# Kernel optimization log

Hardware: AMD Instinct MI355X
Metric: run time of the kernel (lower is better)

## Reference

```python
import jax, jax.numpy as jnp
import numpy as np


def setup_inputs() -> dict:
    key = jax.random.key(0)
    ks = jax.random.split(key, 5)
    b, f, h, w, c = 2, 16, 64, 64, 256
    heads, D = 8, 32
    hD = heads * D
    x = jax.random.normal(ks[0], (b, f, h, w, c), dtype=jnp.float32)
    s = 1.0 / np.sqrt(c)
    Wq = jax.random.normal(ks[1], (c, hD), dtype=jnp.float32) * s
    Wk = jax.random.normal(ks[2], (c, hD), dtype=jnp.float32) * s
    Wv = jax.random.normal(ks[3], (c, hD), dtype=jnp.float32) * s
    Wo = jax.random.normal(ks[4], (hD, c), dtype=jnp.float32) * s
    return {"x": x, "Wq": Wq, "Wk": Wk, "Wv": Wv, "Wo": Wo, "heads": heads}


def reference(x, Wq, Wk, Wv, Wo, heads):
    b, f, h, w, c = x.shape
    hD = Wq.shape[1]
    D = hD // heads
    n = h * w
    # fuse batch & frames; 1x1 conv == channel matmul
    xf = x.reshape(b * f, n, c)  # [(bf), n, c]

    def proj(W):
        # [(bf), n, hD] -> [(bf), heads, D, n]
        p = jnp.einsum('bnc,cd->bnd', xf, W)
        return p.reshape(b * f, n, heads, D).transpose(0, 2, 3, 1)

    q = jax.nn.softmax(proj(Wq), axis=-2)  # softmax over D (note: scale is dead code in source)
    k = jax.nn.softmax(proj(Wk), axis=-1)  # softmax over spatial n
    v = proj(Wv)
    context = jnp.einsum('bhdn,bhen->bhde', k, v)      # [(bf), heads, D, D]
    out = jnp.einsum('bhde,bhdn->bhen', context, q)    # [(bf), heads, D, n]
    out = out.transpose(0, 3, 1, 2).reshape(b * f, n, hD)
    out = jnp.einsum('bnd,dc->bnc', out, Wo)
    return out.reshape(b, f, h, w, c)
```

## Files before the change

kernel.cpp:

```cpp
#include <hip/hip_runtime.h>
#include <hip/hip_bf16.h>


typedef __attribute__((ext_vector_type(8))) short bf16x8;
typedef __attribute__((ext_vector_type(4))) float f32x4;

__device__ __forceinline__ unsigned short f2bf(float x) {
  __hip_bfloat16 h = __float2bfloat16(x);
  union { __hip_bfloat16 b; unsigned short u; } c; c.b = h; return c.u;
}

__global__ __launch_bounds__(256) void k0_prep(const float* __restrict__ Wq,
                                               const float* __restrict__ Wk,
                                               const float* __restrict__ Wv,
                                               unsigned short* __restrict__ WqT,
                                               unsigned short* __restrict__ WkvT) {
  int r = blockIdx.x, c = threadIdx.x;
  if (r < 256)      WqT [(r      )*256 + c] = f2bf(Wq[c*256 + r]);
  else if (r < 512) WkvT[(r - 256)*256 + c] = f2bf(Wk[c*256 + (r-256)]);
  else              WkvT[(r - 256)*256 + c] = f2bf(Wv[c*256 + (r-512)]);
}

__global__ __launch_bounds__(512, 2) void k1p(const float* __restrict__ x,
                                              const unsigned short* __restrict__ WkvT,
                                              float* __restrict__ ctxp) {
  __shared__ unsigned short As[2][32*256];
  __shared__ unsigned short slab[512*32];
  int bid = blockIdx.x;
  size_t rowbase = (size_t)bid * 256;
  int tid = threadIdx.x;
  int lane = tid & 63, wid = tid >> 6;
  int cl = lane & 15, rq = (lane >> 4) << 2, fs = lane >> 4;

  bf16x8 bfr[4][8];
#pragma unroll
  for (int nf = 0; nf < 4; ++nf)
#pragma unroll
    for (int kk = 0; kk < 8; ++kk)
      bfr[nf][kk] = *(const bf16x8*)(WkvT + (size_t)(wid*64 + nf*16 + cl)*256 + kk*32 + fs*8);

  f32x4 c2a = {}, c2b = {}, c2c = {}, c2d = {};
  f32x4 c3a = {}, c3b = {};
  bf16x8 bone;
#pragma unroll
  for (int j = 0; j < 8; ++j) bone[j] = (short)0x3F80;

  int ar = tid >> 5, as_ = tid & 31;
  int aw0 = ar*256 + ((as_ ^ (ar & 7)) << 3);
  int aw1 = (16 + ar)*256 + ((as_ ^ (ar & 7)) << 3);
  const float* ap = x + (rowbase + ar)*256 + as_*8;

  float4 pa0 = *(const float4*)ap;
  float4 pa1 = *(const float4*)(ap + 4);
  float4 pa2 = *(const float4*)(ap + 16*256);
  float4 pa3 = *(const float4*)(ap + 16*256 + 4);

  for (int t = 0; t < 8; ++t) {
    unsigned short* Ab = &As[t & 1][0];
    {
      union { ushort4 u4[2]; int4 i4; } pk;
      pk.u4[0].x = f2bf(pa0.x); pk.u4[0].y = f2bf(pa0.y); pk.u4[0].z = f2bf(pa0.z); pk.u4[0].w = f2bf(pa0.w);
      pk.u4[1].x = f2bf(pa1.x); pk.u4[1].y = f2bf(pa1.y); pk.u4[1].z = f2bf(pa1.z); pk.u4[1].w = f2bf(pa1.w);
      *(int4*)(&Ab[aw0]) = pk.i4;
      pk.u4[0].x = f2bf(pa2.x); pk.u4[0].y = f2bf(pa2.y); pk.u4[0].z = f2bf(pa2.z); pk.u4[0].w = f2bf(pa2.w);
      pk.u4[1].x = f2bf(pa3.x); pk.u4[1].y = f2bf(pa3.y); pk.u4[1].z = f2bf(pa3.z); pk.u4[1].w = f2bf(pa3.w);
      *(int4*)(&Ab[aw1]) = pk.i4;
    }
    __syncthreads();
    if (t < 7) {
      const float* apn = ap + (size_t)(t + 1)*32*256;
      pa0 = *(const float4*)apn;
      pa1 = *(const float4*)(apn + 4);
      pa2 = *(const float4*)(apn + 16*256);
      pa3 = *(const float4*)(apn + 16*256 + 4);
    }
    f32x4 acc0[4] = {};
    f32x4 acc1[4] = {};
#pragma unroll
    for (int kk = 0; kk < 8; ++kk) {
      int so = (((kk*4 + fs) ^ (cl & 7)) << 3);
      bf16x8 a0 = *(const bf16x8*)(&Ab[cl*256 + so]);
      bf16x8 a1 = *(const bf16x8*)(&Ab[(16 + cl)*256 + so]);
#pragma unroll
      for (int ni = 0; ni < 4; ++ni) {
        acc0[ni] = __builtin_amdgcn_mfma_f32_16x16x32_bf16(a0, bfr[ni][kk], acc0[ni], 0, 0, 0);
        acc1[ni] = __builtin_amdgcn_mfma_f32_16x16x32_bf16(a1, bfr[ni][kk], acc1[ni], 0, 0, 0);
      }
    }
#pragma unroll
    for (int ni = 0; ni < 4; ++ni) {
      int c = wid*64 + ni*16 + cl;
      int sw = (c ^ (c >> 2)) & 3;
      ushort4 w0, w1;
      if (wid < 4) {
        w0.x = f2bf(__expf(acc0[ni][0])); w0.y = f2bf(__expf(acc0[ni][1]));
        w0.z = f2bf(__expf(acc0[ni][2])); w0.w = f2bf(__expf(acc0[ni][3]));
        w1.x = f2bf(__expf(acc1[ni][0])); w1.y = f2bf(__expf(acc1[ni][1]));
        w1.z = f2bf(__expf(acc1[ni][2])); w1.w = f2bf(__expf(acc1[ni][3]));
      } else {
        w0.x = f2bf(acc0[ni][0]); w0.y = f2bf(acc0[ni][1]);
        w0.z = f2bf(acc0[ni][2]); w0.w = f2bf(acc0[ni][3]);
        w1.x = f2bf(acc1[ni][0]); w1.y = f2bf(acc1[ni][1]);
        w1.z = f2bf(acc1[ni][2]); w1.w = f2bf(acc1[ni][3]);
      }
      *(ushort4*)(&slab[c*32 + (((rq >> 3) ^ sw) << 3) + (rq & 7)]) = w0;
      *(ushort4*)(&slab[c*32 + ((((16 + rq) >> 3) ^ sw) << 3) + (rq & 7)]) = w1;
    }
    __syncthreads();
    {
      int ca0 = wid*32 + cl,        ca1 = wid*32 + 16 + cl;
      int cb0 = 256 + wid*32 + cl,  cb1 = 256 + wid*32 + 16 + cl;
      bf16x8 af0 = *(const bf16x8*)(&slab[ca0*32 + ((fs ^ ((ca0 ^ (ca0 >> 2)) & 3)) << 3)]);
      bf16x8 af1 = *(const bf16x8*)(&slab[ca1*32 + ((fs ^ ((ca1 ^ (ca1 >> 2)) & 3)) << 3)]);
      bf16x8 bv0 = *(const bf16x8*)(&slab[cb0*32 + ((fs ^ ((cb0 ^ (cb0 >> 2)) & 3)) << 3)]);
      bf16x8 bv1 = *(const bf16x8*)(&slab[cb1*32 + ((fs ^ ((cb1 ^ (cb1 >> 2)) & 3)) << 3)]);
      c2a = __builtin_amdgcn_mfma_f32_16x16x32_bf16(af0, bv0, c2a, 0, 0, 0);
      c2b = __builtin_amdgcn_mfma_f32_16x16x32_bf16(af0, bv1, c2b, 0, 0, 0);
      c2c = __builtin_amdgcn_mfma_f32_16x16x32_bf16(af1, bv0, c2c, 0, 0, 0);
      c2d = __builtin_amdgcn_mfma_f32_16x16x32_bf16(af1, bv1, c2d, 0, 0, 0);
      c3a = __builtin_amdgcn_mfma_f32_16x16x32_bf16(af0, bone, c3a, 0, 0, 0);
      c3b = __builtin_amdgcn_mfma_f32_16x16x32_bf16(af1, bone, c3b, 0, 0, 0);
    }
  }
  float* cp = ctxp + ((size_t)bid*8 + wid)*1056;
#pragma unroll
  for (int r = 0; r < 4; ++r) {
    cp[(rq + r)*33 + cl]            = c2a[r];
    cp[(rq + r)*33 + 16 + cl]       = c2b[r];
    cp[(16 + rq + r)*33 + cl]       = c2c[r];
    cp[(16 + rq + r)*33 + 16 + cl]  = c2d[r];
  }
  if (cl == 0) {
#pragma unroll
    for (int r = 0; r < 4; ++r) {
      cp[(rq + r)*33 + 32]      = c3a[r];
      cp[(16 + rq + r)*33 + 32] = c3b[r];
    }
  }
}

__global__ __launch_bounds__(256) void k2b_w2(const float* __restrict__ ctxp,
                                              const float* __restrict__ Wo,
                                              unsigned short* __restrict__ W2t) {
  __shared__ float clds[32*33];
  int bid = blockIdx.x;
  int h = bid & 7, bfi = bid >> 3;
  int tid = threadIdx.x;
  for (int i = tid; i < 1056; i += 256) {
    float s = 0.f;
#pragma unroll
    for (int p = 0; p < 16; ++p)
      s += ctxp[((size_t)(bfi*16 + p)*8 + h)*1056 + i];
    clds[i] = s;
  }
  __syncthreads();
  float acc[32] = {};
#pragma unroll 4
  for (int e = 0; e < 32; ++e) {
    float w = Wo[(size_t)(h*32 + e)*256 + tid];
#pragma unroll
    for (int d = 0; d < 32; ++d) acc[d] += clds[d*33 + e] * w;
  }
  unsigned short* o = W2t + ((size_t)bfi*256 + tid)*256 + h*32;
#pragma unroll
  for (int d = 0; d < 32; ++d) o[d] = f2bf(acc[d] / clds[d*33 + 32]);
}

__global__ __launch_bounds__(512, 2) void k3s(const float* __restrict__ x,
                                              const unsigned short* __restrict__ WqT,
                                              const unsigned short* __restrict__ W2t,
                                              float* __restrict__ out) {
  __shared__ unsigned short As[2][32*256];
  __shared__ unsigned short Qs[2][32*256];
  int bid = blockIdx.x;
  size_t rowbase = (size_t)bid * 256;
  int bfi = bid >> 4;
  int tid = threadIdx.x;
  int lane = tid & 63, wid = tid >> 6;
  int cl = lane & 15, rq = (lane >> 4) << 2, fs = lane >> 4;

  bf16x8 bq[2][8], bw[2][8];
#pragma unroll
  for (int nf = 0; nf < 2; ++nf)
#pragma unroll
    for (int kk = 0; kk < 8; ++kk) {
      bq[nf][kk] = *(const bf16x8*)(WqT + (size_t)(wid*32 + nf*16 + cl)*256 + kk*32 + fs*8);
      bw[nf][kk] = *(const bf16x8*)(W2t + ((size_t)bfi*256 + wid*32 + nf*16 + cl)*256 + kk*32 + fs*8);
    }

  int ar = tid >> 5, as_ = tid & 31;
  int aw0 = ar*256 + ((as_ ^ (ar & 7)) << 3);
  int aw1 = (16 + ar)*256 + ((as_ ^ (ar & 7)) << 3);
  const float* ap = x + (rowbase + ar)*256 + as_*8;

  int qslotbase = wid*4 + (rq >> 3);
  ushort4 qpk[2][2];

  float4 pa0 = *(const float4*)ap;
  float4 pa1 = *(const float4*)(ap + 4);
  float4 pa2 = *(const float4*)(ap + 16*256);
  float4 pa3 = *(const float4*)(ap + 16*256 + 4);
  {
    unsigned short* Ab = &As[0][0];
    union { ushort4 u4[2]; int4 i4; } pk;
    pk.u4[0].x = f2bf(pa0.x); pk.u4[0].y = f2bf(pa0.y); pk.u4[0].z = f2bf(pa0.z); pk.u4[0].w = f2bf(pa0.w);
    pk.u4[1].x = f2bf(pa1.x); pk.u4[1].y = f2bf(pa1.y); pk.u4[1].z = f2bf(pa1.z); pk.u4[1].w = f2bf(pa1.w);
    *(int4*)(&Ab[aw0]) = pk.i4;
    pk.u4[0].x = f2bf(pa2.x); pk.u4[0].y = f2bf(pa2.y); pk.u4[0].z = f2bf(pa2.z); pk.u4[0].w = f2bf(pa2.w);
    pk.u4[1].x = f2bf(pa3.x); pk.u4[1].y = f2bf(pa3.y); pk.u4[1].z = f2bf(pa3.z); pk.u4[1].w = f2bf(pa3.w);
    *(int4*)(&Ab[aw1]) = pk.i4;
  }
  {
    const float* apn = ap + 32*256;
    pa0 = *(const float4*)apn;
    pa1 = *(const float4*)(apn + 4);
    pa2 = *(const float4*)(apn + 16*256);
    pa3 = *(const float4*)(apn + 16*256 + 4);
  }
  __syncthreads();
  {
    unsigned short* Ab = &As[0][0];
    f32x4 ql[2][2] = {};
#pragma unroll
    for (int kk = 0; kk < 8; ++kk) {
      int so = (((kk*4 + fs) ^ (cl & 7)) << 3);
      bf16x8 a0 = *(const bf16x8*)(&Ab[cl*256 + so]);
      bf16x8 a1 = *(const bf16x8*)(&Ab[(16 + cl)*256 + so]);
#pragma unroll
      for (int nf = 0; nf < 2; ++nf) {
        ql[0][nf] = __builtin_amdgcn_mfma_f32_16x16x32_bf16(bq[nf][kk], a0, ql[0][nf], 0, 0, 0);
        ql[1][nf] = __builtin_amdgcn_mfma_f32_16x16x32_bf16(bq[nf][kk], a1, ql[1][nf], 0, 0, 0);
      }
    }
#pragma unroll
    for (int m = 0; m < 2; ++m) {
      float e0[4], e1[4]; float s8 = 0.f;
#pragma unroll
      for (int r = 0; r < 4; ++r) { e0[r] = __expf(ql[m][0][r]); e1[r] = __expf(ql[m][1][r]); s8 += e0[r] + e1[r]; }
      float s = s8; s += __shfl_xor(s, 16); s += __shfl_xor(s, 32);
      float inv = 1.0f / s;
      qpk[m][0].x = f2bf(e0[0]*inv); qpk[m][0].y = f2bf(e0[1]*inv); qpk[m][0].z = f2bf(e0[2]*inv); qpk[m][0].w = f2bf(e0[3]*inv);
      qpk[m][1].x = f2bf(e1[0]*inv); qpk[m][1].y = f2bf(e1[1]*inv); qpk[m][1].z = f2bf(e1[2]*inv); qpk[m][1].w = f2bf(e1[3]*inv);
    }
  }
  for (int t = 0; t < 7; ++t) {
    {
      unsigned short* Ab = &As[(t + 1) & 1][0];
      union { ushort4 u4[2]; int4 i4; } pk;
      pk.u4[0].x = f2bf(pa0.x); pk.u4[0].y = f2bf(pa0.y); pk.u4[0].z = f2bf(pa0.z); pk.u4[0].w = f2bf(pa0.w);
      pk.u4[1].x = f2bf(pa1.x); pk.u4[1].y = f2bf(pa1.y); pk.u4[1].z = f2bf(pa1.z); pk.u4[1].w = f2bf(pa1.w);
      *(int4*)(&Ab[aw0]) = pk.i4;
      pk.u4[0].x = f2bf(pa2.x); pk.u4[0].y = f2bf(pa2.y); pk.u4[0].z = f2bf(pa2.z); pk.u4[0].w = f2bf(pa2.w);
      pk.u4[1].x = f2bf(pa3.x); pk.u4[1].y = f2bf(pa3.y); pk.u4[1].z = f2bf(pa3.z); pk.u4[1].w = f2bf(pa3.w);
      *(int4*)(&Ab[aw1]) = pk.i4;
    }
    {
      unsigned short* Qb = &Qs[t & 1][0];
#pragma unroll
      for (int m = 0; m < 2; ++m) {
        int row = m*16 + cl;
#pragma unroll
        for (int nf = 0; nf < 2; ++nf) {
          int slot = qslotbase + nf*2;
          *(ushort4*)(&Qb[row*256 + ((slot ^ (row & 7)) << 3) + (rq & 4)]) = qpk[m][nf];
        }
      }
    }
    if (t < 6) {
      const float* apn = ap + (size_t)(t + 2)*32*256;
      pa0 = *(const float4*)apn;
      pa1 = *(const float4*)(apn + 4);
      pa2 = *(const float4*)(apn + 16*256);
      pa3 = *(const float4*)(apn + 16*256 + 4);
    }
    __syncthreads();
    f32x4 oa[2][2] = {};
    {
      unsigned short* Qb = &Qs[t & 1][0];
#pragma unroll
      for (int kk = 0; kk < 8; ++kk) {
        int so = (((kk*4 + fs) ^ (cl & 7)) << 3);
        bf16x8 q0 = *(const bf16x8*)(&Qb[cl*256 + so]);
        bf16x8 q1 = *(const bf16x8*)(&Qb[(16 + cl)*256 + so]);
#pragma unroll
        for (int nf = 0; nf < 2; ++nf) {
          oa[0][nf] = __builtin_amdgcn_mfma_f32_16x16x32_bf16(bw[nf][kk], q0, oa[0][nf], 0, 0, 0);
          oa[1][nf] = __builtin_amdgcn_mfma_f32_16x16x32_bf16(bw[nf][kk], q1, oa[1][nf], 0, 0, 0);
        }
      }
    }
    {
      unsigned short* Ab = &As[(t + 1) & 1][0];
      f32x4 ql[2][2] = {};
#pragma unroll
      for (int kk = 0; kk < 8; ++kk) {
        int so = (((kk*4 + fs) ^ (cl & 7)) << 3);
        bf16x8 a0 = *(const bf16x8*)(&Ab[cl*256 + so]);
        bf16x8 a1 = *(const bf16x8*)(&Ab[(16 + cl)*256 + so]);
#pragma unroll
        for (int nf = 0; nf < 2; ++nf) {
          ql[0][nf] = __builtin_amdgcn_mfma_f32_16x16x32_bf16(bq[nf][kk], a0, ql[0][nf], 0, 0, 0);
          ql[1][nf] = __builtin_amdgcn_mfma_f32_16x16x32_bf16(bq[nf][kk], a1, ql[1][nf], 0, 0, 0);
        }
      }
#pragma unroll
      for (int m = 0; m < 2; ++m) {
        float e0[4], e1[4]; float s8 = 0.f;
#pragma unroll
        for (int r = 0; r < 4; ++r) { e0[r] = __expf(ql[m][0][r]); e1[r] = __expf(ql[m][1][r]); s8 += e0[r] + e1[r]; }
        float s = s8; s += __shfl_xor(s, 16); s += __shfl_xor(s, 32);
        float inv = 1.0f / s;
        qpk[m][0].x = f2bf(e0[0]*inv); qpk[m][0].y = f2bf(e0[1]*inv); qpk[m][0].z = f2bf(e0[2]*inv); qpk[m][0].w = f2bf(e0[3]*inv);
        qpk[m][1].x = f2bf(e1[0]*inv); qpk[m][1].y = f2bf(e1[1]*inv); qpk[m][1].z = f2bf(e1[2]*inv); qpk[m][1].w = f2bf(e1[3]*inv);
      }
    }
#pragma unroll
    for (int m = 0; m < 2; ++m)
#pragma unroll
      for (int nf = 0; nf < 2; ++nf)
        *(f32x4*)(&out[(rowbase + (size_t)t*32 + m*16 + cl)*256 + wid*32 + nf*16 + rq]) = oa[m][nf];
  }
  {
    unsigned short* Qb = &Qs[1][0];
#pragma unroll
    for (int m = 0; m < 2; ++m) {
      int row = m*16 + cl;
#pragma unroll
      for (int nf = 0; nf < 2; ++nf) {
        int slot = qslotbase + nf*2;
        *(ushort4*)(&Qb[row*256 + ((slot ^ (row & 7)) << 3) + (rq & 4)]) = qpk[m][nf];
      }
    }
  }
  __syncthreads();
  {
    unsigned short* Qb = &Qs[1][0];
    f32x4 oa[2][2] = {};
#pragma unroll
    for (int kk = 0; kk < 8; ++kk) {
      int so = (((kk*4 + fs) ^ (cl & 7)) << 3);
      bf16x8 q0 = *(const bf16x8*)(&Qb[cl*256 + so]);
      bf16x8 q1 = *(const bf16x8*)(&Qb[(16 + cl)*256 + so]);
#pragma unroll
      for (int nf = 0; nf < 2; ++nf) {
        oa[0][nf] = __builtin_amdgcn_mfma_f32_16x16x32_bf16(bw[nf][kk], q0, oa[0][nf], 0, 0, 0);
        oa[1][nf] = __builtin_amdgcn_mfma_f32_16x16x32_bf16(bw[nf][kk], q1, oa[1][nf], 0, 0, 0);
      }
    }
#pragma unroll
    for (int m = 0; m < 2; ++m)
#pragma unroll
      for (int nf = 0; nf < 2; ++nf)
        *(f32x4*)(&out[(rowbase + (size_t)7*32 + m*16 + cl)*256 + wid*32 + nf*16 + rq]) = oa[m][nf];
  }
}

extern "C" void kernel_launch(void* const* d_in, const int* in_sizes, int n_in,
                              void* d_out, int out_size, void* d_ws, size_t ws_size,
                              hipStream_t stream) {
  const float* x  = (const float*)d_in[0];
  const float* Wq = (const float*)d_in[1];
  const float* Wk = (const float*)d_in[2];
  const float* Wv = (const float*)d_in[3];
  const float* Wo = (const float*)d_in[4];
  float* out = (float*)d_out;

  unsigned short* WkvT = (unsigned short*)d_ws;
  unsigned short* WqT  = WkvT + 131072;
  unsigned short* W2t  = WqT  + 65536;
  float*          ctxp = (float*)(W2t + 2097152);

  k0_prep <<<768,  256, 0, stream>>>(Wq, Wk, Wv, WqT, WkvT);
  k1p     <<<512,  512, 0, stream>>>(x, WkvT, ctxp);
  k2b_w2  <<<256,  256, 0, stream>>>(ctxp, Wo, W2t);
  k3s     <<<512,  512, 0, stream>>>(x, WqT, W2t, out);
}
```

Measured before the change: 141.9 us.

## Software-pipeline k1p with double-buffered slab and one barrier per step

Measured after the change: 142.8 us. Within noise of the previous version (+0.6%).

```diff
diff --git a/kernel.cpp b/kernel.cpp
--- a/kernel.cpp
+++ b/kernel.cpp
@@ -25,7 +25,7 @@
                                               const unsigned short* __restrict__ WkvT,
                                               float* __restrict__ ctxp) {
   __shared__ unsigned short As[2][32*256];
-  __shared__ unsigned short slab[512*32];
+  __shared__ unsigned short slab[2][512*32];
   int bid = blockIdx.x;
   size_t rowbase = (size_t)bid * 256;
   int tid = threadIdx.x;
@@ -50,14 +50,79 @@
   int aw1 = (16 + ar)*256 + ((as_ ^ (ar & 7)) << 3);
   const float* ap = x + (rowbase + ar)*256 + as_*8;
 
+  int ca0 = wid*32 + cl,        ca1 = wid*32 + 16 + cl;
+  int cb0 = 256 + wid*32 + cl,  cb1 = 256 + wid*32 + 16 + cl;
+  int ra0 = ca0*32 + ((fs ^ ((ca0 ^ (ca0 >> 2)) & 3)) << 3);
+  int ra1 = ca1*32 + ((fs ^ ((ca1 ^ (ca1 >> 2)) & 3)) << 3);
+  int rb0 = cb0*32 + ((fs ^ ((cb0 ^ (cb0 >> 2)) & 3)) << 3);
+  int rb1 = cb1*32 + ((fs ^ ((cb1 ^ (cb1 >> 2)) & 3)) << 3);
+
+  f32x4 acc0[4], acc1[4];
+
   float4 pa0 = *(const float4*)ap;
   float4 pa1 = *(const float4*)(ap + 4);
   float4 pa2 = *(const float4*)(ap + 16*256);
   float4 pa3 = *(const float4*)(ap + 16*256 + 4);
-
-  for (int t = 0; t < 8; ++t) {
-    unsigned short* Ab = &As[t & 1][0];
-    {
+  {
+    unsigned short* Ab = &As[0][0];
+    union { ushort4 u4[2]; int4 i4; } pk;
+    pk.u4[0].x = f2bf(pa0.x); pk.u4[0].y = f2bf(pa0.y); pk.u4[0].z = f2bf(pa0.z); pk.u4[0].w = f2bf(pa0.w);
+    pk.u4[1].x = f2bf(pa1.x); pk.u4[1].y = f2bf(pa1.y); pk.u4[1].z = f2bf(pa1.z); pk.u4[1].w = f2bf(pa1.w);
+    *(int4*)(&Ab[aw0]) = pk.i4;
+    pk.u4[0].x = f2bf(pa2.x); pk.u4[0].y = f2bf(pa2.y); pk.u4[0].z = f2bf(pa2.z); pk.u4[0].w = f2bf(pa2.w);
+    pk.u4[1].x = f2bf(pa3.x); pk.u4[1].y = f2bf(pa3.y); pk.u4[1].z = f2bf(pa3.z); pk.u4[1].w = f2bf(pa3.w);
+    *(int4*)(&Ab[aw1]) = pk.i4;
+  }
+  {
+    const float* apn = ap + 32*256;
+    pa0 = *(const float4*)apn;
+    pa1 = *(const float4*)(apn + 4);
+    pa2 = *(const float4*)(apn + 16*256);
+    pa3 = *(const float4*)(apn + 16*256 + 4);
+  }
+  __syncthreads();
+  {
+    unsigned short* Ab = &As[0][0];
+#pragma unroll
+    for (int ni = 0; ni < 4; ++ni) { acc0[ni] = (f32x4){}; acc1[ni] = (f32x4){}; }
+#pragma unroll
+    for (int kk = 0; kk < 8; ++kk) {
+      int so = (((kk*4 + fs) ^ (cl & 7)) << 3);
+      bf16x8 a0 = *(const bf16x8*)(&Ab[cl*256 + so]);
+      bf16x8 a1 = *(const bf16x8*)(&Ab[(16 + cl)*256 + so]);
+#pragma unroll
+      for (int ni = 0; ni < 4; ++ni) {
+        acc0[ni] = __builtin_amdgcn_mfma_f32_16x16x32_bf16(a0, bfr[ni][kk], acc0[ni], 0, 0, 0);
+        acc1[ni] = __builtin_amdgcn_mfma_f32_16x16x32_bf16(a1, bfr[ni][kk], acc1[ni], 0, 0, 0);
+      }
+    }
+  }
+
+  for (int t = 0; t < 7; ++t) {
+    {
+      unsigned short* sb = &slab[t & 1][0];
+#pragma unroll
+      for (int ni = 0; ni < 4; ++ni) {
+        int c = wid*64 + ni*16 + cl;
+        int sw = (c ^ (c >> 2)) & 3;
+        ushort4 w0, w1;
+        if (wid < 4) {
+          w0.x = f2bf(__expf(acc0[ni][0])); w0.y = f2bf(__expf(acc0[ni][1]));
+          w0.z = f2bf(__expf(acc0[ni][2])); w0.w = f2bf(__expf(acc0[ni][3]));
+          w1.x = f2bf(__expf(acc1[ni][0])); w1.y = f2bf(__expf(acc1[ni][1]));
+          w1.z = f2bf(__expf(acc1[ni][2])); w1.w = f2bf(__expf(acc1[ni][3]));
+        } else {
+          w0.x = f2bf(acc0[ni][0]); w0.y = f2bf(acc0[ni][1]);
+          w0.z = f2bf(acc0[ni][2]); w0.w = f2bf(acc0[ni][3]);
+          w1.x = f2bf(acc1[ni][0]); w1.y = f2bf(acc1[ni][1]);
+          w1.z = f2bf(acc1[ni][2]); w1.w = f2bf(acc1[ni][3]);
+        }
+        *(ushort4*)(&sb[c*32 + (((rq >> 3) ^ sw) << 3) + (rq & 7)]) = w0;
+        *(ushort4*)(&sb[c*32 + ((((16 + rq) >> 3) ^ sw) << 3) + (rq & 7)]) = w1;
+      }
+    }
+    {
+      unsigned short* Ab = &As[(t + 1) & 1][0];
       union { ushort4 u4[2]; int4 i4; } pk;
       pk.u4[0].x = f2bf(pa0.x); pk.u4[0].y = f2bf(pa0.y); pk.u4[0].z = f2bf(pa0.z); pk.u4[0].w = f2bf(pa0.w);
       pk.u4[1].x = f2bf(pa1.x); pk.u4[1].y = f2bf(pa1.y); pk.u4[1].z = f2bf(pa1.z); pk.u4[1].w = f2bf(pa1.w);
@@ -66,27 +131,46 @@
       pk.u4[1].x = f2bf(pa3.x); pk.u4[1].y = f2bf(pa3.y); pk.u4[1].z = f2bf(pa3.z); pk.u4[1].w = f2bf(pa3.w);
       *(int4*)(&Ab[aw1]) = pk.i4;
     }
-    __syncthreads();
-    if (t < 7) {
-      const float* apn = ap + (size_t)(t + 1)*32*256;
+    if (t < 6) {
+      const float* apn = ap + (size_t)(t + 2)*32*256;
       pa0 = *(const float4*)apn;
       pa1 = *(const float4*)(apn + 4);
       pa2 = *(const float4*)(apn + 16*256);
       pa3 = *(const float4*)(apn + 16*256 + 4);
     }
-    f32x4 acc0[4] = {};
-    f32x4 acc1[4] = {};
-#pragma unroll
-    for (int kk = 0; kk < 8; ++kk) {
-      int so = (((kk*4 + fs) ^ (cl & 7)) << 3);
-      bf16x8 a0 = *(const bf16x8*)(&Ab[cl*256 + so]);
-      bf16x8 a1 = *(const bf16x8*)(&Ab[(16 + cl)*256 + so]);
-#pragma unroll
-      for (int ni = 0; ni < 4; ++ni) {
-        acc0[ni] = __builtin_amdgcn_mfma_f32_16x16x32_bf16(a0, bfr[ni][kk], acc0[ni], 0, 0, 0);
-        acc1[ni] = __builtin_amdgcn_mfma_f32_16x16x32_bf16(a1, bfr[ni][kk], acc1[ni], 0, 0, 0);
-      }
-    }
+    __syncthreads();
+    {
+      unsigned short* sb = &slab[t & 1][0];
+      bf16x8 af0 = *(const bf16x8*)(&sb[ra0]);
+      bf16x8 af1 = *(const bf16x8*)(&sb[ra1]);
+      bf16x8 bv0 = *(const bf16x8*)(&sb[rb0]);
+      bf16x8 bv1 = *(const bf16x8*)(&sb[rb1]);
+      c2a = __builtin_amdgcn_mfma_f32_16x16x32_bf16(af0, bv0, c2a, 0, 0, 0);
+      c2b = __builtin_amdgcn_mfma_f32_16x16x32_bf16(af0, bv1, c2b, 0, 0, 0);
+      c2c = __builtin_amdgcn_mfma_f32_16x16x32_bf16(af1, bv0, c2c, 0, 0, 0);
+      c2d = __builtin_amdgcn_mfma_f32_16x16x32_bf16(af1, bv1, c2d, 0, 0, 0);
+      c3a = __builtin_amdgcn_mfma_f32_16x16x32_bf16(af0, bone, c3a, 0, 0, 0);
+      c3b = __builtin_amdgcn_mfma_f32_16x16x32_bf16(af1, bone, c3b, 0, 0, 0);
+    }
+    {
+      unsigned short* Ab = &As[(t + 1) & 1][0];
+#pragma unroll
+      for (int ni = 0; ni < 4; ++ni) { acc0[ni] = (f32x4){}; acc1[ni] = (f32x4){}; }
+#pragma unroll
+      for (int kk = 0; kk < 8; ++kk) {
+        int so = (((kk*4 + fs) ^ (cl & 7)) << 3);
+        bf16x8 a0 = *(const bf16x8*)(&Ab[cl*256 + so]);
+        bf16x8 a1 = *(const bf16x8*)(&Ab[(16 + cl)*256 + so]);
+#pragma unroll
+        for (int ni = 0; ni < 4; ++ni) {
+          acc0[ni] = __builtin_amdgcn_mfma_f32_16x16x32_bf16(a0, bfr[ni][kk], acc0[ni], 0, 0, 0);
+          acc1[ni] = __builtin_amdgcn_mfma_f32_16x16x32_bf16(a1, bfr[ni][kk], acc1[ni], 0, 0, 0);
+        }
+      }
+    }
+  }
+  {
+    unsigned short* sb = &slab[1][0];
 #pragma unroll
     for (int ni = 0; ni < 4; ++ni) {
       int c = wid*64 + ni*16 + cl;
@@ -103,24 +187,23 @@
         w1.x = f2bf(acc1[ni][0]); w1.y = f2bf(acc1[ni][1]);
         w1.z = f2bf(acc1[ni][2]); w1.w = f2bf(acc1[ni][3]);
       }
-      *(ushort4*)(&slab[c*32 + (((rq >> 3) ^ sw) << 3) + (rq & 7)]) = w0;
-      *(ushort4*)(&slab[c*32 + ((((16 + rq) >> 3) ^ sw) << 3) + (rq & 7)]) = w1;
-    }
-    __syncthreads();
-    {
-      int ca0 = wid*32 + cl,        ca1 = wid*32 + 16 + cl;
-      int cb0 = 256 + wid*32 + cl,  cb1 = 256 + wid*32 + 16 + cl;
-      bf16x8 af0 = *(const bf16x8*)(&slab[ca0*32 + ((fs ^ ((ca0 ^ (ca0 >> 2)) & 3)) << 3)]);
-      bf16x8 af1 = *(const bf16x8*)(&slab[ca1*32 + ((fs ^ ((ca1 ^ (ca1 >> 2)) & 3)) << 3)]);
-      bf16x8 bv0 = *(const bf16x8*)(&slab[cb0*32 + ((fs ^ ((cb0 ^ (cb0 >> 2)) & 3)) << 3)]);
-      bf16x8 bv1 = *(const bf16x8*)(&slab[cb1*32 + ((fs ^ ((cb1 ^ (cb1 >> 2)) & 3)) << 3)]);
-      c2a = __builtin_amdgcn_mfma_f32_16x16x32_bf16(af0, bv0, c2a, 0, 0, 0);
-      c2b = __builtin_amdgcn_mfma_f32_16x16x32_bf16(af0, bv1, c2b, 0, 0, 0);
-      c2c = __builtin_amdgcn_mfma_f32_16x16x32_bf16(af1, bv0, c2c, 0, 0, 0);
-      c2d = __builtin_amdgcn_mfma_f32_16x16x32_bf16(af1, bv1, c2d, 0, 0, 0);
-      c3a = __builtin_amdgcn_mfma_f32_16x16x32_bf16(af0, bone, c3a, 0, 0, 0);
-      c3b = __builtin_amdgcn_mfma_f32_16x16x32_bf16(af1, bone, c3b, 0, 0, 0);
-    }
+      *(ushort4*)(&sb[c*32 + (((rq >> 3) ^ sw) << 3) + (rq & 7)]) = w0;
+      *(ushort4*)(&sb[c*32 + ((((16 + rq) >> 3) ^ sw) << 3) + (rq & 7)]) = w1;
+    }
+  }
+  __syncthreads();
+  {
+    unsigned short* sb = &slab[1][0];
+    bf16x8 af0 = *(const bf16x8*)(&sb[ra0]);
+    bf16x8 af1 = *(const bf16x8*)(&sb[ra1]);
+    bf16x8 bv0 = *(const bf16x8*)(&sb[rb0]);
+    bf16x8 bv1 = *(const bf16x8*)(&sb[rb1]);
+    c2a = __builtin_amdgcn_mfma_f32_16x16x32_bf16(af0, bv0, c2a, 0, 0, 0);
+    c2b = __builtin_amdgcn_mfma_f32_16x16x32_bf16(af0, bv1, c2b, 0, 0, 0);
+    c2c = __builtin_amdgcn_mfma_f32_16x16x32_bf16(af1, bv0, c2c, 0, 0, 0);
+    c2d = __builtin_amdgcn_mfma_f32_16x16x32_bf16(af1, bv1, c2d, 0, 0, 0);
+    c3a = __builtin_amdgcn_mfma_f32_16x16x32_bf16(af0, bone, c3a, 0, 0, 0);
+    c3b = __builtin_amdgcn_mfma_f32_16x16x32_bf16(af1, bone, c3b, 0, 0, 0);
   }
   float* cp = ctxp + ((size_t)bid*8 + wid)*1056;
 #pragma unroll
```

## Split K/V projection across heads, cache bf16 x for Q pass via LDS DMA

Applied to the files above, without the earlier changes.

Measured after the change: 202.1 us. 1.42x slower.

```diff
diff --git a/kernel.cpp b/kernel.cpp
--- a/kernel.cpp
+++ b/kernel.cpp
@@ -8,6 +8,11 @@
 __device__ __forceinline__ unsigned short f2bf(float x) {
   __hip_bfloat16 h = __float2bfloat16(x);
   union { __hip_bfloat16 b; unsigned short u; } c; c.b = h; return c.u;
+}
+
+__device__ __forceinline__ void gl16(const unsigned short* g, unsigned short* l) {
+  __builtin_amdgcn_global_load_lds((const __attribute__((address_space(1))) void*)g,
+                                   (__attribute__((address_space(3))) void*)l, 16, 0, 0);
 }
 
 __global__ __launch_bounds__(256) void k0_prep(const float* __restrict__ Wq,
@@ -21,120 +26,148 @@
   else              WkvT[(r - 256)*256 + c] = f2bf(Wv[c*256 + (r-512)]);
 }
 
-__global__ __launch_bounds__(512, 2) void k1p(const float* __restrict__ x,
+__global__ __launch_bounds__(512, 4) void k1x(const float* __restrict__ x,
                                               const unsigned short* __restrict__ WkvT,
-                                              float* __restrict__ ctxp) {
+                                              float* __restrict__ ctxp,
+                                              unsigned short* __restrict__ XB) {
   __shared__ unsigned short As[2][32*256];
-  __shared__ unsigned short slab[512*32];
+  __shared__ unsigned short slab[2][256*32];
   int bid = blockIdx.x;
-  size_t rowbase = (size_t)bid * 256;
+  int rc = bid & 511, hb = bid >> 9;
+  size_t rowbase = (size_t)rc * 256;
   int tid = threadIdx.x;
-  int lane = tid & 63, wid = tid >> 6;
+  int lane = tid & 63, w = tid >> 6;
   int cl = lane & 15, rq = (lane >> 4) << 2, fs = lane >> 4;
-
-  bf16x8 bfr[4][8];
-#pragma unroll
-  for (int nf = 0; nf < 4; ++nf)
+  bool isE = w < 4;
+  int wb = isE ? hb*128 + w*32 : 256 + hb*128 + (w - 4)*32;
+
+  bf16x8 bfr[2][8];
+#pragma unroll
+  for (int ni = 0; ni < 2; ++ni)
 #pragma unroll
     for (int kk = 0; kk < 8; ++kk)
-      bfr[nf][kk] = *(const bf16x8*)(WkvT + (size_t)(wid*64 + nf*16 + cl)*256 + kk*32 + fs*8);
-
-  f32x4 c2a = {}, c2b = {}, c2c = {}, c2d = {};
-  f32x4 c3a = {}, c3b = {};
-  bf16x8 bone;
-#pragma unroll
-  for (int j = 0; j < 8; ++j) bone[j] = (short)0x3F80;
+      bfr[ni][kk] = *(const bf16x8*)(WkvT + (size_t)(wb + ni*16 + cl)*256 + kk*32 + fs*8);
+
+  int hl = w >> 1, dh = w & 1;
+  f32x4 c2[2] = {};
+  float dena0 = 0.f, dena1 = 0.f;
 
   int ar = tid >> 5, as_ = tid & 31;
   int aw0 = ar*256 + ((as_ ^ (ar & 7)) << 3);
   int aw1 = (16 + ar)*256 + ((as_ ^ (ar & 7)) << 3);
   const float* ap = x + (rowbase + ar)*256 + as_*8;
-
-  float4 pa0 = *(const float4*)ap;
-  float4 pa1 = *(const float4*)(ap + 4);
-  float4 pa2 = *(const float4*)(ap + 16*256);
-  float4 pa3 = *(const float4*)(ap + 16*256 + 4);
-
-  for (int t = 0; t < 8; ++t) {
-    unsigned short* Ab = &As[t & 1][0];
-    {
-      union { ushort4 u4[2]; int4 i4; } pk;
-      pk.u4[0].x = f2bf(pa0.x); pk.u4[0].y = f2bf(pa0.y); pk.u4[0].z = f2bf(pa0.z); pk.u4[0].w = f2bf(pa0.w);
-      pk.u4[1].x = f2bf(pa1.x); pk.u4[1].y = f2bf(pa1.y); pk.u4[1].z = f2bf(pa1.z); pk.u4[1].w = f2bf(pa1.w);
-      *(int4*)(&Ab[aw0]) = pk.i4;
-      pk.u4[0].x = f2bf(pa2.x); pk.u4[0].y = f2bf(pa2.y); pk.u4[0].z = f2bf(pa2.z); pk.u4[0].w = f2bf(pa2.w);
-      pk.u4[1].x = f2bf(pa3.x); pk.u4[1].y = f2bf(pa3.y); pk.u4[1].z = f2bf(pa3.z); pk.u4[1].w = f2bf(pa3.w);
-      *(int4*)(&Ab[aw1]) = pk.i4;
-    }
-    __syncthreads();
-    if (t < 7) {
-      const float* apn = ap + (size_t)(t + 1)*32*256;
-      pa0 = *(const float4*)apn;
-      pa1 = *(const float4*)(apn + 4);
-      pa2 = *(const float4*)(apn + 16*256);
-      pa3 = *(const float4*)(apn + 16*256 + 4);
-    }
-    f32x4 acc0[4] = {};
-    f32x4 acc1[4] = {};
+  unsigned short* xbp = XB + (rowbase + ar)*256 + as_*8;
+
+  int ca  = hl*32 + dh*16 + cl;
+  int cb0 = 128 + hl*32 + cl, cb1 = cb0 + 16;
+  int ra  = ca*32  + ((fs ^ ((ca ^ (ca >> 2)) & 3)) << 3);
+  int rb0 = cb0*32 + ((fs ^ ((cb0 ^ (cb0 >> 2)) & 3)) << 3);
+  int rb1 = cb1*32 + ((fs ^ ((cb1 ^ (cb1 >> 2)) & 3)) << 3);
+
+  f32x4 acc[2][2];
+  float4 pa0, pa1, pa2, pa3;
+
+  auto loadpa = [&](int ts) {
+    const float* p = ap + (size_t)ts*32*256;
+    pa0 = *(const float4*)p;
+    pa1 = *(const float4*)(p + 4);
+    pa2 = *(const float4*)(p + 16*256);
+    pa3 = *(const float4*)(p + 16*256 + 4);
+  };
+  auto stage = [&](int buf, int ts) {
+    unsigned short* Ab = &As[buf][0];
+    union { ushort4 u4[2]; int4 i4; } pk;
+    pk.u4[0].x = f2bf(pa0.x); pk.u4[0].y = f2bf(pa0.y); pk.u4[0].z = f2bf(pa0.z); pk.u4[0].w = f2bf(pa0.w);
+    pk.u4[1].x = f2bf(pa1.x); pk.u4[1].y = f2bf(pa1.y); pk.u4[1].z = f2bf(pa1.z); pk.u4[1].w = f2bf(pa1.w);
+    *(int4*)(&Ab[aw0]) = pk.i4;
+    if (hb == 0) *(int4*)(xbp + (size_t)ts*8192) = pk.i4;
+    pk.u4[0].x = f2bf(pa2.x); pk.u4[0].y = f2bf(pa2.y); pk.u4[0].z = f2bf(pa2.z); pk.u4[0].w = f2bf(pa2.w);
+    pk.u4[1].x = f2bf(pa3.x); pk.u4[1].y = f2bf(pa3.y); pk.u4[1].z = f2bf(pa3.z); pk.u4[1].w = f2bf(pa3.w);
+    *(int4*)(&Ab[aw1]) = pk.i4;
+    if (hb == 0) *(int4*)(xbp + (size_t)ts*8192 + 4096) = pk.i4;
+  };
+  auto mainmfma = [&](int buf) {
+    unsigned short* Ab = &As[buf][0];
+#pragma unroll
+    for (int m = 0; m < 2; ++m)
+#pragma unroll
+      for (int ni = 0; ni < 2; ++ni) acc[m][ni] = (f32x4){};
 #pragma unroll
     for (int kk = 0; kk < 8; ++kk) {
       int so = (((kk*4 + fs) ^ (cl & 7)) << 3);
       bf16x8 a0 = *(const bf16x8*)(&Ab[cl*256 + so]);
       bf16x8 a1 = *(const bf16x8*)(&Ab[(16 + cl)*256 + so]);
 #pragma unroll
-      for (int ni = 0; ni < 4; ++ni) {
-        acc0[ni] = __builtin_amdgcn_mfma_f32_16x16x32_bf16(a0, bfr[ni][kk], acc0[ni], 0, 0, 0);
-        acc1[ni] = __builtin_amdgcn_mfma_f32_16x16x32_bf16(a1, bfr[ni][kk], acc1[ni], 0, 0, 0);
-      }
-    }
-#pragma unroll
-    for (int ni = 0; ni < 4; ++ni) {
-      int c = wid*64 + ni*16 + cl;
+      for (int ni = 0; ni < 2; ++ni) {
+        acc[0][ni] = __builtin_amdgcn_mfma_f32_16x16x32_bf16(a0, bfr[ni][kk], acc[0][ni], 0, 0, 0);
+        acc[1][ni] = __builtin_amdgcn_mfma_f32_16x16x32_bf16(a1, bfr[ni][kk], acc[1][ni], 0, 0, 0);
+      }
+    }
+  };
+  auto slabwrite = [&](int buf) {
+    unsigned short* sb = &slab[buf][0];
+#pragma unroll
+    for (int ni = 0; ni < 2; ++ni) {
+      int c = w*32 + ni*16 + cl;
       int sw = (c ^ (c >> 2)) & 3;
-      ushort4 w0, w1;
-      if (wid < 4) {
-        w0.x = f2bf(__expf(acc0[ni][0])); w0.y = f2bf(__expf(acc0[ni][1]));
-        w0.z = f2bf(__expf(acc0[ni][2])); w0.w = f2bf(__expf(acc0[ni][3]));
-        w1.x = f2bf(__expf(acc1[ni][0])); w1.y = f2bf(__expf(acc1[ni][1]));
-        w1.z = f2bf(__expf(acc1[ni][2])); w1.w = f2bf(__expf(acc1[ni][3]));
-      } else {
-        w0.x = f2bf(acc0[ni][0]); w0.y = f2bf(acc0[ni][1]);
-        w0.z = f2bf(acc0[ni][2]); w0.w = f2bf(acc0[ni][3]);
-        w1.x = f2bf(acc1[ni][0]); w1.y = f2bf(acc1[ni][1]);
-        w1.z = f2bf(acc1[ni][2]); w1.w = f2bf(acc1[ni][3]);
-      }
-      *(ushort4*)(&slab[c*32 + (((rq >> 3) ^ sw) << 3) + (rq & 7)]) = w0;
-      *(ushort4*)(&slab[c*32 + ((((16 + rq) >> 3) ^ sw) << 3) + (rq & 7)]) = w1;
-    }
+#pragma unroll
+      for (int m = 0; m < 2; ++m) {
+        int n4 = m*16 + rq;
+        ushort4 wv;
+        if (isE) {
+          float e0 = __expf(acc[m][ni][0]), e1 = __expf(acc[m][ni][1]);
+          float e2 = __expf(acc[m][ni][2]), e3 = __expf(acc[m][ni][3]);
+          if (ni == 0) dena0 += (e0 + e1) + (e2 + e3); else dena1 += (e0 + e1) + (e2 + e3);
+          wv.x = f2bf(e0); wv.y = f2bf(e1); wv.z = f2bf(e2); wv.w = f2bf(e3);
+        } else {
+          wv.x = f2bf(acc[m][ni][0]); wv.y = f2bf(acc[m][ni][1]);
+          wv.z = f2bf(acc[m][ni][2]); wv.w = f2bf(acc[m][ni][3]);
+        }
+        *(ushort4*)(&sb[c*32 + (((n4 >> 3) ^ sw) << 3) + (n4 & 7)]) = wv;
+      }
+    }
+  };
+  auto ctxmfma = [&](int buf) {
+    unsigned short* sb = &slab[buf][0];
+    bf16x8 af  = *(const bf16x8*)(&sb[ra]);
+    bf16x8 bv0 = *(const bf16x8*)(&sb[rb0]);
+    bf16x8 bv1 = *(const bf16x8*)(&sb[rb1]);
+    c2[0] = __builtin_amdgcn_mfma_f32_16x16x32_bf16(af, bv0, c2[0], 0, 0, 0);
+    c2[1] = __builtin_amdgcn_mfma_f32_16x16x32_bf16(af, bv1, c2[1], 0, 0, 0);
+  };
+
+  loadpa(0);
+  stage(0, 0);
+  loadpa(1);
+  __syncthreads();
+  mainmfma(0);
+
+  for (int t = 0; t < 7; ++t) {
+    slabwrite(t & 1);
+    stage((t + 1) & 1, t + 1);
+    if (t < 6) loadpa(t + 2);
     __syncthreads();
-    {
-      int ca0 = wid*32 + cl,        ca1 = wid*32 + 16 + cl;
-      int cb0 = 256 + wid*32 + cl,  cb1 = 256 + wid*32 + 16 + cl;
-      bf16x8 af0 = *(const bf16x8*)(&slab[ca0*32 + ((fs ^ ((ca0 ^ (ca0 >> 2)) & 3)) << 3)]);
-      bf16x8 af1 = *(const bf16x8*)(&slab[ca1*32 + ((fs ^ ((ca1 ^ (ca1 >> 2)) & 3)) << 3)]);
-      bf16x8 bv0 = *(const bf16x8*)(&slab[cb0*32 + ((fs ^ ((cb0 ^ (cb0 >> 2)) & 3)) << 3)]);
-      bf16x8 bv1 = *(const bf16x8*)(&slab[cb1*32 + ((fs ^ ((cb1 ^ (cb1 >> 2)) & 3)) << 3)]);
-      c2a = __builtin_amdgcn_mfma_f32_16x16x32_bf16(af0, bv0, c2a, 0, 0, 0);
-      c2b = __builtin_amdgcn_mfma_f32_16x16x32_bf16(af0, bv1, c2b, 0, 0, 0);
-      c2c = __builtin_amdgcn_mfma_f32_16x16x32_bf16(af1, bv0, c2c, 0, 0, 0);
-      c2d = __builtin_amdgcn_mfma_f32_16x16x32_bf16(af1, bv1, c2d, 0, 0, 0);
-      c3a = __builtin_amdgcn_mfma_f32_16x16x32_bf16(af0, bone, c3a, 0, 0, 0);
-      c3b = __builtin_amdgcn_mfma_f32_16x16x32_bf16(af1, bone, c3b, 0, 0, 0);
-    }
-  }
-  float* cp = ctxp + ((size_t)bid*8 + wid)*1056;
-#pragma unroll
-  for (int r = 0; r < 4; ++r) {
-    cp[(rq + r)*33 + cl]            = c2a[r];
-    cp[(rq + r)*33 + 16 + cl]       = c2b[r];
-    cp[(16 + rq + r)*33 + cl]       = c2c[r];
-    cp[(16 + rq + r)*33 + 16 + cl]  = c2d[r];
-  }
-  if (cl == 0) {
-#pragma unroll
-    for (int r = 0; r < 4; ++r) {
-      cp[(rq + r)*33 + 32]      = c3a[r];
-      cp[(16 + rq + r)*33 + 32] = c3b[r];
+    ctxmfma(t & 1);
+    mainmfma((t + 1) & 1);
+  }
+  slabwrite(1);
+  __syncthreads();
+  ctxmfma(1);
+
+  int hgl = hb*4 + hl;
+  float* cp = ctxp + ((size_t)rc*8 + hgl)*1056;
+#pragma unroll
+  for (int eh = 0; eh < 2; ++eh)
+#pragma unroll
+    for (int r = 0; r < 4; ++r)
+      cp[(dh*16 + rq + r)*33 + eh*16 + cl] = c2[eh][r];
+  if (isE) {
+    dena0 += __shfl_xor(dena0, 16); dena0 += __shfl_xor(dena0, 32);
+    dena1 += __shfl_xor(dena1, 16); dena1 += __shfl_xor(dena1, 32);
+    float* cpd = ctxp + ((size_t)rc*8 + hb*4 + w)*1056;
+    if (fs == 0) {
+      cpd[cl*33 + 32]        = dena0;
+      cpd[(16 + cl)*33 + 32] = dena1;
     }
   }
 }
@@ -166,7 +199,7 @@
   for (int d = 0; d < 32; ++d) o[d] = f2bf(acc[d] / clds[d*33 + 32]);
 }
 
-__global__ __launch_bounds__(512, 2) void k3s(const float* __restrict__ x,
+__global__ __launch_bounds__(512, 2) void k3x(const unsigned short* __restrict__ XB,
                                               const unsigned short* __restrict__ WqT,
                                               const unsigned short* __restrict__ W2t,
                                               float* __restrict__ out) {
@@ -188,38 +221,19 @@
       bw[nf][kk] = *(const bf16x8*)(W2t + ((size_t)bfi*256 + wid*32 + nf*16 + cl)*256 + kk*32 + fs*8);
     }
 
-  int ar = tid >> 5, as_ = tid & 31;
-  int aw0 = ar*256 + ((as_ ^ (ar & 7)) << 3);
-  int aw1 = (16 + ar)*256 + ((as_ ^ (ar & 7)) << 3);
-  const float* ap = x + (rowbase + ar)*256 + as_*8;
+  int sr = tid >> 5, ss = tid & 31;
+  const unsigned short* xs0 = XB + (rowbase + sr)*256 + ((ss ^ (sr & 7)) << 3);
+  const unsigned short* xs1 = xs0 + 16*256;
 
   int qslotbase = wid*4 + (rq >> 3);
   ushort4 qpk[2][2];
 
-  float4 pa0 = *(const float4*)ap;
-  float4 pa1 = *(const float4*)(ap + 4);
-  float4 pa2 = *(const float4*)(ap + 16*256);
-  float4 pa3 = *(const float4*)(ap + 16*256 + 4);
-  {
-    unsigned short* Ab = &As[0][0];
-    union { ushort4 u4[2]; int4 i4; } pk;
-    pk.u4[0].x = f2bf(pa0.x); pk.u4[0].y = f2bf(pa0.y); pk.u4[0].z = f2bf(pa0.z); pk.u4[0].w = f2bf(pa0.w);
-    pk.u4[1].x = f2bf(pa1.x); pk.u4[1].y = f2bf(pa1.y); pk.u4[1].z = f2bf(pa1.z); pk.u4[1].w = f2bf(pa1.w);
-    *(int4*)(&Ab[aw0]) = pk.i4;
-    pk.u4[0].x = f2bf(pa2.x); pk.u4[0].y = f2bf(pa2.y); pk.u4[0].z = f2bf(pa2.z); pk.u4[0].w = f2bf(pa2.w);
-    pk.u4[1].x = f2bf(pa3.x); pk.u4[1].y = f2bf(pa3.y); pk.u4[1].z = f2bf(pa3.z); pk.u4[1].w = f2bf(pa3.w);
-    *(int4*)(&Ab[aw1]) = pk.i4;
-  }
-  {
-    const float* apn = ap + 32*256;
-    pa0 = *(const float4*)apn;
-    pa1 = *(const float4*)(apn + 4);
-    pa2 = *(const float4*)(apn + 16*256);
-    pa3 = *(const float4*)(apn + 16*256 + 4);
-  }
-  __syncthreads();
-  {
-    unsigned short* Ab = &As[0][0];
+  auto stageA = [&](int buf, int ts) {
+    gl16(xs0 + (size_t)ts*8192, &As[buf][(wid*64)*8]);
+    gl16(xs1 + (size_t)ts*8192, &As[buf][(512 + wid*64)*8]);
+  };
+  auto p1soft = [&](int buf) {
+    unsigned short* Ab = &As[buf][0];
     f32x4 ql[2][2] = {};
 #pragma unroll
     for (int kk = 0; kk < 8; ++kk) {
@@ -242,37 +256,27 @@
       qpk[m][0].x = f2bf(e0[0]*inv); qpk[m][0].y = f2bf(e0[1]*inv); qpk[m][0].z = f2bf(e0[2]*inv); qpk[m][0].w = f2bf(e0[3]*inv);
       qpk[m][1].x = f2bf(e1[0]*inv); qpk[m][1].y = f2bf(e1[1]*inv); qpk[m][1].z = f2bf(e1[2]*inv); qpk[m][1].w = f2bf(e1[3]*inv);
     }
-  }
+  };
+  auto qwrite = [&](int buf) {
+    unsigned short* Qb = &Qs[buf][0];
+#pragma unroll
+    for (int m = 0; m < 2; ++m) {
+      int row = m*16 + cl;
+#pragma unroll
+      for (int nf = 0; nf < 2; ++nf) {
+        int slot = qslotbase + nf*2;
+        *(ushort4*)(&Qb[row*256 + ((slot ^ (row & 7)) << 3) + (rq & 4)]) = qpk[m][nf];
+      }
+    }
+  };
+
+  stageA(0, 0);
+  __syncthreads();
+  p1soft(0);
+
   for (int t = 0; t < 7; ++t) {
-    {
-      unsigned short* Ab = &As[(t + 1) & 1][0];
-      union { ushort4 u4[2]; int4 i4; } pk;
-      pk.u4[0].x = f2bf(pa0.x); pk.u4[0].y = f2bf(pa0.y); pk.u4[0].z = f2bf(pa0.z); pk.u4[0].w = f2bf(pa0.w);
-      pk.u4[1].x = f2bf(pa1.x); pk.u4[1].y = f2bf(pa1.y); pk.u4[1].z = f2bf(pa1.z); pk.u4[1].w = f2bf(pa1.w);
-      *(int4*)(&Ab[aw0]) = pk.i4;
-      pk.u4[0].x = f2bf(pa2.x); pk.u4[0].y = f2bf(pa2.y); pk.u4[0].z = f2bf(pa2.z); pk.u4[0].w = f2bf(pa2.w);
-      pk.u4[1].x = f2bf(pa3.x); pk.u4[1].y = f2bf(pa3.y); pk.u4[1].z = f2bf(pa3.z); pk.u4[1].w = f2bf(pa3.w);
-      *(int4*)(&Ab[aw1]) = pk.i4;
-    }
-    {
-      unsigned short* Qb = &Qs[t & 1][0];
-#pragma unroll
-      for (int m = 0; m < 2; ++m) {
-        int row = m*16 + cl;
-#pragma unroll
-        for (int nf = 0; nf < 2; ++nf) {
-          int slot = qslotbase + nf*2;
-          *(ushort4*)(&Qb[row*256 + ((slot ^ (row & 7)) << 3) + (rq & 4)]) = qpk[m][nf];
-        }
-      }
-    }
-    if (t < 6) {
-      const float* apn = ap + (size_t)(t + 2)*32*256;
-      pa0 = *(const float4*)apn;
-      pa1 = *(const float4*)(apn + 4);
-      pa2 = *(const float4*)(apn + 16*256);
-      pa3 = *(const float4*)(apn + 16*256 + 4);
-    }
+    stageA((t + 1) & 1, t + 1);
+    qwrite(t & 1);
     __syncthreads();
     f32x4 oa[2][2] = {};
     {
@@ -289,49 +293,14 @@
         }
       }
     }
-    {
-      unsigned short* Ab = &As[(t + 1) & 1][0];
-      f32x4 ql[2][2] = {};
-#pragma unroll
-      for (int kk = 0; kk < 8; ++kk) {
-        int so = (((kk*4 + fs) ^ (cl & 7)) << 3);
-        bf16x8 a0 = *(const bf16x8*)(&Ab[cl*256 + so]);
-        bf16x8 a1 = *(const bf16x8*)(&Ab[(16 + cl)*256 + so]);
-#pragma unroll
-        for (int nf = 0; nf < 2; ++nf) {
-          ql[0][nf] = __builtin_amdgcn_mfma_f32_16x16x32_bf16(bq[nf][kk], a0, ql[0][nf], 0, 0, 0);
-          ql[1][nf] = __builtin_amdgcn_mfma_f32_16x16x32_bf16(bq[nf][kk], a1, ql[1][nf], 0, 0, 0);
-        }
-      }
-#pragma unroll
-      for (int m = 0; m < 2; ++m) {
-        float e0[4], e1[4]; float s8 = 0.f;
-#pragma unroll
-        for (int r = 0; r < 4; ++r) { e0[r] = __expf(ql[m][0][r]); e1[r] = __expf(ql[m][1][r]); s8 += e0[r] + e1[r]; }
-        float s = s8; s += __shfl_xor(s, 16); s += __shfl_xor(s, 32);
-        float inv = 1.0f / s;
-        qpk[m][0].x = f2bf(e0[0]*inv); qpk[m][0].y = f2bf(e0[1]*inv); qpk[m][0].z = f2bf(e0[2]*inv); qpk[m][0].w = f2bf(e0[3]*inv);
-        qpk[m][1].x = f2bf(e1[0]*inv); qpk[m][1].y = f2bf(e1[1]*inv); qpk[m][1].z = f2bf(e1[2]*inv); qpk[m][1].w = f2bf(e1[3]*inv);
-      }
-    }
+    p1soft((t + 1) & 1);
 #pragma unroll
     for (int m = 0; m < 2; ++m)
 #pragma unroll
       for (int nf = 0; nf < 2; ++nf)
         *(f32x4*)(&out[(rowbase + (size_t)t*32 + m*16 + cl)*256 + wid*32 + nf*16 + rq]) = oa[m][nf];
   }
-  {
-    unsigned short* Qb = &Qs[1][0];
-#pragma unroll
-    for (int m = 0; m < 2; ++m) {
-      int row = m*16 + cl;
-#pragma unroll
-      for (int nf = 0; nf < 2; ++nf) {
-        int slot = qslotbase + nf*2;
-        *(ushort4*)(&Qb[row*256 + ((slot ^ (row & 7)) << 3) + (rq & 4)]) = qpk[m][nf];
-      }
-    }
-  }
+  qwrite(1);
   __syncthreads();
   {
     unsigned short* Qb = &Qs[1][0];
@@ -369,9 +338,10 @@
   unsigned short* WqT  = WkvT + 131072;
   unsigned short* W2t  = WqT  + 65536;
   float*          ctxp = (float*)(W2t + 2097152);
+  unsigned short* XB   = (unsigned short*)(ctxp + (size_t)512*8*1056);
 
   k0_prep <<<768,  256, 0, stream>>>(Wq, Wk, Wv, WqT, WkvT);
-  k1p     <<<512,  512, 0, stream>>>(x, WkvT, ctxp);
+  k1x     <<<1024, 512, 0, stream>>>(x, WkvT, ctxp, XB);
   k2b_w2  <<<256,  256, 0, stream>>>(ctxp, Wo, W2t);
-  k3s     <<<512,  512, 0, stream>>>(x, WqT, W2t, out);
-}
+  k3x     <<<512,  512, 0, stream>>>(XB, WqT, W2t, out);
+}
```
